# Performance work log

Measured on AMD Instinct MI355X. Metric: run time of the kernel, lower is better.

Reference implementation:

```python
import jax, jax.numpy as jnp
import numpy as np
import math

N_EMBD = 64
HEAD_SIZE = 64
B, T = 16, 2048


def setup_inputs() -> dict:
    key = jax.random.key(0)
    k1, k2, k3, k4 = jax.random.split(key, 4)
    inputs = jax.random.normal(k1, (B, T, N_EMBD), dtype=jnp.float32)
    # Causal mask: True where attention is NOT allowed (upper triangle),
    # matching masked_fill_(mask, -1e9) with mask = ~tril.
    mask = jnp.triu(jnp.ones((T, T), dtype=bool), k=1)
    # nn.Linear(n_embd, head_size, bias=False) weights, stored as
    # (n_embd, head_size) so projection is inputs @ W (== x @ W_torch.T).
    scale = 1.0 / math.sqrt(N_EMBD)
    Wq = jax.random.uniform(k2, (N_EMBD, HEAD_SIZE), jnp.float32, -scale, scale)
    Wk = jax.random.uniform(k3, (N_EMBD, HEAD_SIZE), jnp.float32, -scale, scale)
    Wv = jax.random.uniform(k4, (N_EMBD, HEAD_SIZE), jnp.float32, -scale, scale)
    return {"inputs": inputs, "mask": mask, "Wq": Wq, "Wk": Wk, "Wv": Wv}


def reference(inputs, mask, Wq, Wk, Wv):
    # inputs: (B, T, n_embd); mask: (T, T) bool broadcast over batch
    q = inputs @ Wq  # (B, T, H)
    k = inputs @ Wk  # (B, T, H)
    v = inputs @ Wv  # (B, T, H)
    inv_sqrt_h = 1.0 / math.sqrt(HEAD_SIZE)
    scores = jnp.einsum('bth,bsh->bts', q, k) * inv_sqrt_h  # (B, T, T)
    scores = jnp.where(mask, jnp.float32(-1e9), scores)
    attention = jax.nn.softmax(scores, axis=-1)
    out = jnp.einsum('bts,bsh->bth', attention, v)  # (B, T, H)
    return out
```

## Files before the change

### kernel.cpp

```cpp
#include <hip/hip_runtime.h>
#include <stdint.h>


typedef __bf16 bf16x8 __attribute__((ext_vector_type(8)));
typedef __bf16 bf16x4 __attribute__((ext_vector_type(4)));
typedef float f32x4 __attribute__((ext_vector_type(4)));

#define QSCALE 0.18033688011112042f

__device__ __forceinline__ unsigned short f2bf(float f) {
  union { float f; unsigned u; } x; x.f = f;
  unsigned r = x.u + 0x7fffu + ((x.u >> 16) & 1u);
  return (unsigned short)(r >> 16);
}

__device__ __forceinline__ int swz(int row, int bytecol) {
  return row * 128 + (bytecol ^ ((row & 7) << 4));
}
__device__ __forceinline__ bf16x8 frag(const unsigned short* base, int row, int kf, int lane) {
  int off = swz(row, kf * 64 + ((lane >> 4) << 4));
  return *(const bf16x8*)((const char*)base + off);
}

__global__ __launch_bounds__(256, 3) void proj_kernel(
    const float* __restrict__ X, const float* __restrict__ Wq,
    const float* __restrict__ Wk, const float* __restrict__ Wv,
    unsigned short* __restrict__ Qg, unsigned short* __restrict__ Kg,
    unsigned short* __restrict__ Vtg) {
  __shared__ __align__(16) unsigned short Xs[128 * 64];
  __shared__ __align__(16) unsigned short Ws[64 * 64];
  const int tid = threadIdx.x, lane = tid & 63, w = tid >> 6;
  const int mat = blockIdx.y;
  const long grow0 = (long)blockIdx.x * 128;

  for (int c = tid; c < 1024; c += 256) {
    int r = c >> 3, cc = c & 7;
    const float* src = X + (grow0 + r) * 64 + cc * 8;
    float4 f0 = *(const float4*)src;
    float4 f1 = *(const float4*)(src + 4);
    uint4 d;
    d.x = f2bf(f0.x) | ((unsigned)f2bf(f0.y) << 16);
    d.y = f2bf(f0.z) | ((unsigned)f2bf(f0.w) << 16);
    d.z = f2bf(f1.x) | ((unsigned)f2bf(f1.y) << 16);
    d.w = f2bf(f1.z) | ((unsigned)f2bf(f1.w) << 16);
    *(uint4*)((char*)Xs + swz(r, cc * 16)) = d;
  }
  const float* wsrc = (mat == 0) ? Wq : (mat == 1) ? Wk : Wv;
  for (int c = tid; c < 4096; c += 256) {
    int e = c >> 6, hh = c & 63;
    *(unsigned short*)((char*)Ws + swz(hh, e * 2)) = f2bf(wsrc[c]);
  }
  __syncthreads();

  const f32x4 zero = {0.f, 0.f, 0.f, 0.f};
  const int mrowb = w * 32;

  bf16x8 xf[2][2];
#pragma unroll
  for (int s = 0; s < 2; ++s)
#pragma unroll
    for (int kf = 0; kf < 2; ++kf)
      xf[s][kf] = frag(Xs, mrowb + s * 16 + (lane & 15), kf, lane);

  if (mat < 2) {
    unsigned short* dst = mat ? Kg : Qg;
#pragma unroll
    for (int s = 0; s < 2; ++s) {
#pragma unroll
      for (int nt = 0; nt < 4; ++nt) {
        bf16x8 b0 = frag(Ws, nt * 16 + (lane & 15), 0, lane);
        bf16x8 b1 = frag(Ws, nt * 16 + (lane & 15), 1, lane);
        f32x4 acc = __builtin_amdgcn_mfma_f32_16x16x32_bf16(xf[s][0], b0, zero, 0, 0, 0);
        acc = __builtin_amdgcn_mfma_f32_16x16x32_bf16(xf[s][1], b1, acc, 0, 0, 0);
        long row0 = grow0 + mrowb + s * 16 + ((lane >> 4) << 2);
        int col = nt * 16 + (lane & 15);
#pragma unroll
        for (int i = 0; i < 4; ++i) {
          float v = acc[i];
          if (mat == 0) v *= QSCALE;
          dst[(row0 + i) * 64 + col] = f2bf(v);
        }
      }
    }
  } else {
    const int b = (int)(grow0 >> 11);
    const int tin0 = (int)(grow0 & 2047);
#pragma unroll
    for (int mt = 0; mt < 4; ++mt) {
      bf16x8 a0 = frag(Ws, mt * 16 + (lane & 15), 0, lane);
      bf16x8 a1 = frag(Ws, mt * 16 + (lane & 15), 1, lane);
#pragma unroll
      for (int s = 0; s < 2; ++s) {
        f32x4 acc = __builtin_amdgcn_mfma_f32_16x16x32_bf16(a0, xf[s][0], zero, 0, 0, 0);
        acc = __builtin_amdgcn_mfma_f32_16x16x32_bf16(a1, xf[s][1], acc, 0, 0, 0);
        int t = tin0 + mrowb + s * 16 + (lane & 15);
        int h0 = mt * 16 + ((lane >> 4) << 2);
#pragma unroll
        for (int i = 0; i < 4; ++i)
          Vtg[((long)(b * 64 + h0 + i)) * 2048 + t] = f2bf(acc[i]);
      }
    }
  }
}

__global__ __launch_bounds__(256, 2) void attn5_kernel(
    const unsigned short* __restrict__ Qg, const unsigned short* __restrict__ Kg,
    const unsigned short* __restrict__ Vtg, float* __restrict__ Og) {
  __shared__ __align__(16) unsigned char smem[35840];

  const int bid = blockIdx.x;
  const int slot = bid >> 3;
  const int b = ((bid & 7) << 1) + (slot & 1);
  const int m = slot >> 1;
  const int qt = (slot & 1) ? (31 - m) : m;
  const int q0 = qt * 64;
  const int ns = qt + 1;

  const int tid = threadIdx.x;
  const int lane = tid & 63, w = tid >> 6;
  const int g = lane >> 4, ln = lane & 15;
  const int h = w & 1, qh = w >> 1;

  const unsigned short* qrow = Qg + ((long)b * 2048 + q0 + qh * 32) * 64;
  const bf16x8 qb00 = *(const bf16x8*)(qrow + ln * 64 + g * 8);
  const bf16x8 qb01 = *(const bf16x8*)(qrow + ln * 64 + 32 + g * 8);
  const bf16x8 qb10 = *(const bf16x8*)(qrow + (16 + ln) * 64 + g * 8);
  const bf16x8 qb11 = *(const bf16x8*)(qrow + (16 + ln) * 64 + 32 + g * 8);

  const unsigned short* kbase = Kg + (long)b * 2048 * 64;
  const unsigned short* vbase = Vtg + (long)b * 64 * 2048;

  const int sr = tid >> 2;
  const int sc = tid & 3;

  const f32x4 zero = {0.f, 0.f, 0.f, 0.f};
  f32x4 o0[4], o1[4];
#pragma unroll
  for (int nt = 0; nt < 4; ++nt) { o0[nt] = zero; o1[nt] = zero; }
  float den0 = 0.f, den1 = 0.f;

  {
    const unsigned short* kg = kbase + (long)sr * 64 + sc * 16;
    uint4 k0 = *(const uint4*)kg;
    uint4 k1 = *(const uint4*)(kg + 8);
    const unsigned short* vg = vbase + (long)sr * 2048 + sc * 16;
    uint4 v0 = *(const uint4*)vg;
    uint4 v1 = *(const uint4*)(vg + 8);
    unsigned short* Kb = (unsigned short*)smem;
    unsigned short* Vb = (unsigned short*)(smem + 8192);
    *(uint4*)((char*)Kb + swz(sr, sc * 32)) = k0;
    *(uint4*)((char*)Kb + swz(sr, sc * 32 + 16)) = k1;
    *(uint4*)((char*)Vb + swz(sr, sc * 32)) = v0;
    *(uint4*)((char*)Vb + swz(sr, sc * 32 + 16)) = v1;
  }
  __syncthreads();

  int cur = 0;
  for (int t = 0; t < ns; ++t) {
    const int kv0 = t * 64;
    const bool pre = (t + 1 < ns);
    uint4 k0, k1, v0, v1;
    if (pre) {
      const int kv0n = kv0 + 64;
      const unsigned short* kg = kbase + (long)(kv0n + sr) * 64 + sc * 16;
      k0 = *(const uint4*)kg;
      k1 = *(const uint4*)(kg + 8);
      const unsigned short* vg = vbase + (long)sr * 2048 + kv0n + sc * 16;
      v0 = *(const uint4*)vg;
      v1 = *(const uint4*)(vg + 8);
    }

    const unsigned short* Kb = (const unsigned short*)(smem + cur * 16384);
    const unsigned short* Vb = (const unsigned short*)(smem + cur * 16384 + 8192);

    bf16x8 ka00 = frag(Kb, h * 32 + ln,      0, lane);
    bf16x8 ka01 = frag(Kb, h * 32 + ln,      1, lane);
    bf16x8 ka10 = frag(Kb, h * 32 + 16 + ln, 0, lane);
    bf16x8 ka11 = frag(Kb, h * 32 + 16 + ln, 1, lane);

    bf16x8 vb[4];
#pragma unroll
    for (int nt = 0; nt < 4; ++nt) {
      int row = nt * 16 + ln;
      bf16x4 lo = *(const bf16x4*)((const char*)Vb + swz(row, h * 64 + g * 8));
      bf16x4 hi = *(const bf16x4*)((const char*)Vb + swz(row, h * 64 + 32 + g * 8));
      vb[nt] = __builtin_shufflevector(lo, hi, 0, 1, 2, 3, 4, 5, 6, 7);
    }

    __builtin_amdgcn_s_setprio(1);
    f32x4 st00 = __builtin_amdgcn_mfma_f32_16x16x32_bf16(ka00, qb00, zero, 0, 0, 0);
    st00 = __builtin_amdgcn_mfma_f32_16x16x32_bf16(ka01, qb01, st00, 0, 0, 0);
    f32x4 st01 = __builtin_amdgcn_mfma_f32_16x16x32_bf16(ka00, qb10, zero, 0, 0, 0);
    st01 = __builtin_amdgcn_mfma_f32_16x16x32_bf16(ka01, qb11, st01, 0, 0, 0);
    f32x4 st10 = __builtin_amdgcn_mfma_f32_16x16x32_bf16(ka10, qb00, zero, 0, 0, 0);
    st10 = __builtin_amdgcn_mfma_f32_16x16x32_bf16(ka11, qb01, st10, 0, 0, 0);
    f32x4 st11 = __builtin_amdgcn_mfma_f32_16x16x32_bf16(ka10, qb10, zero, 0, 0, 0);
    st11 = __builtin_amdgcn_mfma_f32_16x16x32_bf16(ka11, qb11, st11, 0, 0, 0);
    __builtin_amdgcn_s_setprio(0);

    if (t == ns - 1) {
      const int qg0 = q0 + qh * 32 + ln;
      const int qg1 = qg0 + 16;
      const int kvb = kv0 + h * 32 + g * 4;
#pragma unroll
      for (int i = 0; i < 4; ++i) {
        if (kvb + i > qg0)      st00[i] = -1e30f;
        if (kvb + i > qg1)      st01[i] = -1e30f;
        if (kvb + 16 + i > qg0) st10[i] = -1e30f;
        if (kvb + 16 + i > qg1) st11[i] = -1e30f;
      }
    }

    bf16x8 pa0, pa1;
#pragma unroll
    for (int i = 0; i < 4; ++i) {
      float p00 = exp2f(st00[i]);
      float p10 = exp2f(st10[i]);
      float p01 = exp2f(st01[i]);
      float p11 = exp2f(st11[i]);
      den0 += p00 + p10;
      den1 += p01 + p11;
      pa0[i] = (__bf16)p00;  pa0[4 + i] = (__bf16)p10;
      pa1[i] = (__bf16)p01;  pa1[4 + i] = (__bf16)p11;
    }

    __builtin_amdgcn_s_setprio(1);
#pragma unroll
    for (int nt = 0; nt < 4; ++nt) {
      o0[nt] = __builtin_amdgcn_mfma_f32_16x16x32_bf16(pa0, vb[nt], o0[nt], 0, 0, 0);
      o1[nt] = __builtin_amdgcn_mfma_f32_16x16x32_bf16(pa1, vb[nt], o1[nt], 0, 0, 0);
    }
    __builtin_amdgcn_s_setprio(0);

    if (pre) {
      unsigned short* Kn = (unsigned short*)(smem + (cur ^ 1) * 16384);
      unsigned short* Vn = (unsigned short*)(smem + (cur ^ 1) * 16384 + 8192);
      *(uint4*)((char*)Kn + swz(sr, sc * 32)) = k0;
      *(uint4*)((char*)Kn + swz(sr, sc * 32 + 16)) = k1;
      *(uint4*)((char*)Vn + swz(sr, sc * 32)) = v0;
      *(uint4*)((char*)Vn + swz(sr, sc * 32 + 16)) = v1;
    }
    __syncthreads();
    cur ^= 1;
  }

  den0 += __shfl_xor(den0, 16);
  den0 += __shfl_xor(den0, 32);
  den1 += __shfl_xor(den1, 16);
  den1 += __shfl_xor(den1, 32);

  float* Olds = (float*)smem;
  float* Dlds = (float*)(smem + 34816);
#pragma unroll
  for (int nt = 0; nt < 4; ++nt)
#pragma unroll
    for (int i = 0; i < 4; ++i) {
      Olds[(h * 64 + qh * 32 + g * 4 + i) * 68 + nt * 16 + ln] = o0[nt][i];
      Olds[(h * 64 + qh * 32 + 16 + g * 4 + i) * 68 + nt * 16 + ln] = o1[nt][i];
    }
  if (lane < 16) {
    Dlds[h * 64 + qh * 32 + ln] = den0;
    Dlds[h * 64 + qh * 32 + 16 + ln] = den1;
  }
  __syncthreads();

  const int q = tid >> 2;
  const int d0 = (tid & 3) * 16;
  float dd = Dlds[q] + Dlds[64 + q];
  float inv = 1.0f / dd;
  float acc[16];
#pragma unroll
  for (int e = 0; e < 16; ++e)
    acc[e] = (Olds[q * 68 + d0 + e] + Olds[(64 + q) * 68 + d0 + e]) * inv;
  float* outp = Og + ((long)b * 2048 + q0 + q) * 64 + d0;
#pragma unroll
  for (int v4 = 0; v4 < 4; ++v4)
    *(float4*)(outp + v4 * 4) = make_float4(acc[v4 * 4], acc[v4 * 4 + 1],
                                            acc[v4 * 4 + 2], acc[v4 * 4 + 3]);
}

extern "C" void kernel_launch(void* const* d_in, const int* in_sizes, int n_in,
                              void* d_out, int out_size, void* d_ws, size_t ws_size,
                              hipStream_t stream) {
  const float* X  = (const float*)d_in[0];
  const float* Wq = (const float*)d_in[2];
  const float* Wk = (const float*)d_in[3];
  const float* Wv = (const float*)d_in[4];

  unsigned short* Qg  = (unsigned short*)d_ws;
  unsigned short* Kg  = Qg + 2097152;
  unsigned short* Vtg = Kg + 2097152;

  proj_kernel<<<dim3(256, 3), 256, 0, stream>>>(X, Wq, Wk, Wv, Qg, Kg, Vtg);
  attn5_kernel<<<512, 256, 0, stream>>>(Qg, Kg, Vtg, (float*)d_out);
}
```

Baseline: 45.71 us.

## Widen attention KV tiles to 128 with 8 warps; fuse Q/K/V projections per block

The attention kernel now runs 512 threads per block. It stages 128-key K/V tiles, double-buffered in a 64KB LDS region, and splits each tile into four 32-key slices across warps. A two-phase LDS reduction combines the four partial outputs and denominators. This halves the number of loop iterations and barriers per query tile and adds warps to hide latency. The cost is more LDS per block, which may limit occupancy, and extra fully masked work on the last tile. The projection kernel now loads each 64-row X tile once and computes Q, K and V from it, instead of launching one block per matrix and reloading X for each.

```diff
diff --git a/kernel.cpp b/kernel.cpp
--- a/kernel.cpp
+++ b/kernel.cpp
@@ -7,6 +7,7 @@
 typedef float f32x4 __attribute__((ext_vector_type(4)));
 
 #define QSCALE 0.18033688011112042f
+#define MFMA16(a, b, c) __builtin_amdgcn_mfma_f32_16x16x32_bf16((a), (b), (c), 0, 0, 0)
 
 __device__ __forceinline__ unsigned short f2bf(float f) {
   union { float f; unsigned u; } x; x.f = f;
@@ -17,109 +18,115 @@
 __device__ __forceinline__ int swz(int row, int bytecol) {
   return row * 128 + (bytecol ^ ((row & 7) << 4));
 }
+__device__ __forceinline__ int swzV(int row, int bytecol) {
+  return row * 256 + (bytecol ^ ((row & 7) << 4));
+}
 __device__ __forceinline__ bf16x8 frag(const unsigned short* base, int row, int kf, int lane) {
   int off = swz(row, kf * 64 + ((lane >> 4) << 4));
   return *(const bf16x8*)((const char*)base + off);
 }
 
-__global__ __launch_bounds__(256, 3) void proj_kernel(
+__global__ __launch_bounds__(256, 2) void proj_kernel(
     const float* __restrict__ X, const float* __restrict__ Wq,
     const float* __restrict__ Wk, const float* __restrict__ Wv,
     unsigned short* __restrict__ Qg, unsigned short* __restrict__ Kg,
     unsigned short* __restrict__ Vtg) {
-  __shared__ __align__(16) unsigned short Xs[128 * 64];
-  __shared__ __align__(16) unsigned short Ws[64 * 64];
+  __shared__ __align__(16) unsigned short Xs[64 * 64];
+  __shared__ __align__(16) unsigned short Ws[3 * 64 * 64];
   const int tid = threadIdx.x, lane = tid & 63, w = tid >> 6;
-  const int mat = blockIdx.y;
-  const long grow0 = (long)blockIdx.x * 128;
-
-  for (int c = tid; c < 1024; c += 256) {
-    int r = c >> 3, cc = c & 7;
-    const float* src = X + (grow0 + r) * 64 + cc * 8;
+  const int ln = lane & 15, g = lane >> 4;
+  const long grow0 = (long)blockIdx.x * 64;
+  const int b = (int)(grow0 >> 11);
+  const int tin0 = (int)(grow0 & 2047);
+
+  {
+    const int r = tid >> 2, c = tid & 3;
+    const float* src = X + (grow0 + r) * 64 + c * 16;
     float4 f0 = *(const float4*)src;
     float4 f1 = *(const float4*)(src + 4);
-    uint4 d;
-    d.x = f2bf(f0.x) | ((unsigned)f2bf(f0.y) << 16);
-    d.y = f2bf(f0.z) | ((unsigned)f2bf(f0.w) << 16);
-    d.z = f2bf(f1.x) | ((unsigned)f2bf(f1.y) << 16);
-    d.w = f2bf(f1.z) | ((unsigned)f2bf(f1.w) << 16);
-    *(uint4*)((char*)Xs + swz(r, cc * 16)) = d;
-  }
-  const float* wsrc = (mat == 0) ? Wq : (mat == 1) ? Wk : Wv;
-  for (int c = tid; c < 4096; c += 256) {
-    int e = c >> 6, hh = c & 63;
-    *(unsigned short*)((char*)Ws + swz(hh, e * 2)) = f2bf(wsrc[c]);
+    float4 f2 = *(const float4*)(src + 8);
+    float4 f3 = *(const float4*)(src + 12);
+    uint4 d0, d1;
+    d0.x = f2bf(f0.x) | ((unsigned)f2bf(f0.y) << 16);
+    d0.y = f2bf(f0.z) | ((unsigned)f2bf(f0.w) << 16);
+    d0.z = f2bf(f1.x) | ((unsigned)f2bf(f1.y) << 16);
+    d0.w = f2bf(f1.z) | ((unsigned)f2bf(f1.w) << 16);
+    d1.x = f2bf(f2.x) | ((unsigned)f2bf(f2.y) << 16);
+    d1.y = f2bf(f2.z) | ((unsigned)f2bf(f2.w) << 16);
+    d1.z = f2bf(f3.x) | ((unsigned)f2bf(f3.y) << 16);
+    d1.w = f2bf(f3.z) | ((unsigned)f2bf(f3.w) << 16);
+    *(uint4*)((char*)Xs + swz(r, c * 32)) = d0;
+    *(uint4*)((char*)Xs + swz(r, c * 32 + 16)) = d1;
+  }
+  for (int c = tid; c < 3 * 4096; c += 256) {
+    const int mat = c >> 12, rr = c & 4095;
+    const int e = rr >> 6, hh = rr & 63;
+    const float* wsrc = (mat == 0) ? Wq : (mat == 1) ? Wk : Wv;
+    *(unsigned short*)((char*)(Ws + mat * 4096) + swz(hh, e * 2)) = f2bf(wsrc[rr]);
   }
   __syncthreads();
 
   const f32x4 zero = {0.f, 0.f, 0.f, 0.f};
-  const int mrowb = w * 32;
-
-  bf16x8 xf[2][2];
-#pragma unroll
-  for (int s = 0; s < 2; ++s)
-#pragma unroll
-    for (int kf = 0; kf < 2; ++kf)
-      xf[s][kf] = frag(Xs, mrowb + s * 16 + (lane & 15), kf, lane);
-
-  if (mat < 2) {
-    unsigned short* dst = mat ? Kg : Qg;
-#pragma unroll
-    for (int s = 0; s < 2; ++s) {
+#pragma unroll
+  for (int i = 0; i < 3; ++i) {
+    const int task = w * 3 + i;
+    const int mat = task >> 2, s = task & 3;
+    const unsigned short* wbase = Ws + mat * 4096;
+    if (mat < 2) {
+      bf16x8 a0 = frag(Xs, s * 16 + ln, 0, lane);
+      bf16x8 a1 = frag(Xs, s * 16 + ln, 1, lane);
+      unsigned short* dst = mat ? Kg : Qg;
 #pragma unroll
       for (int nt = 0; nt < 4; ++nt) {
-        bf16x8 b0 = frag(Ws, nt * 16 + (lane & 15), 0, lane);
-        bf16x8 b1 = frag(Ws, nt * 16 + (lane & 15), 1, lane);
-        f32x4 acc = __builtin_amdgcn_mfma_f32_16x16x32_bf16(xf[s][0], b0, zero, 0, 0, 0);
-        acc = __builtin_amdgcn_mfma_f32_16x16x32_bf16(xf[s][1], b1, acc, 0, 0, 0);
-        long row0 = grow0 + mrowb + s * 16 + ((lane >> 4) << 2);
-        int col = nt * 16 + (lane & 15);
-#pragma unroll
-        for (int i = 0; i < 4; ++i) {
-          float v = acc[i];
+        bf16x8 b0 = frag(wbase, nt * 16 + ln, 0, lane);
+        bf16x8 b1 = frag(wbase, nt * 16 + ln, 1, lane);
+        f32x4 acc = MFMA16(a0, b0, zero);
+        acc = MFMA16(a1, b1, acc);
+        long row0 = grow0 + s * 16 + g * 4;
+        int col = nt * 16 + ln;
+#pragma unroll
+        for (int k = 0; k < 4; ++k) {
+          float v = acc[k];
           if (mat == 0) v *= QSCALE;
-          dst[(row0 + i) * 64 + col] = f2bf(v);
+          dst[(row0 + k) * 64 + col] = f2bf(v);
         }
       }
-    }
-  } else {
-    const int b = (int)(grow0 >> 11);
-    const int tin0 = (int)(grow0 & 2047);
-#pragma unroll
-    for (int mt = 0; mt < 4; ++mt) {
-      bf16x8 a0 = frag(Ws, mt * 16 + (lane & 15), 0, lane);
-      bf16x8 a1 = frag(Ws, mt * 16 + (lane & 15), 1, lane);
-#pragma unroll
-      for (int s = 0; s < 2; ++s) {
-        f32x4 acc = __builtin_amdgcn_mfma_f32_16x16x32_bf16(a0, xf[s][0], zero, 0, 0, 0);
-        acc = __builtin_amdgcn_mfma_f32_16x16x32_bf16(a1, xf[s][1], acc, 0, 0, 0);
-        int t = tin0 + mrowb + s * 16 + (lane & 15);
-        int h0 = mt * 16 + ((lane >> 4) << 2);
-#pragma unroll
-        for (int i = 0; i < 4; ++i)
-          Vtg[((long)(b * 64 + h0 + i)) * 2048 + t] = f2bf(acc[i]);
+    } else {
+      bf16x8 a0 = frag(wbase, s * 16 + ln, 0, lane);
+      bf16x8 a1 = frag(wbase, s * 16 + ln, 1, lane);
+#pragma unroll
+      for (int nt = 0; nt < 4; ++nt) {
+        bf16x8 b0 = frag(Xs, nt * 16 + ln, 0, lane);
+        bf16x8 b1 = frag(Xs, nt * 16 + ln, 1, lane);
+        f32x4 acc = MFMA16(a0, b0, zero);
+        acc = MFMA16(a1, b1, acc);
+        int t = tin0 + nt * 16 + ln;
+        int h0 = s * 16 + g * 4;
+#pragma unroll
+        for (int k = 0; k < 4; ++k)
+          Vtg[((long)(b * 64 + h0 + k)) * 2048 + t] = f2bf(acc[k]);
       }
     }
   }
 }
 
-__global__ __launch_bounds__(256, 2) void attn5_kernel(
+__global__ __launch_bounds__(512, 4) void attn7_kernel(
     const unsigned short* __restrict__ Qg, const unsigned short* __restrict__ Kg,
     const unsigned short* __restrict__ Vtg, float* __restrict__ Og) {
-  __shared__ __align__(16) unsigned char smem[35840];
+  __shared__ __align__(16) unsigned char smem[65536];
 
   const int bid = blockIdx.x;
-  const int slot = bid >> 3;
-  const int b = ((bid & 7) << 1) + (slot & 1);
-  const int m = slot >> 1;
-  const int qt = (slot & 1) ? (31 - m) : m;
+  const int xcd = bid & 7, idx = bid >> 3;
+  const int b = (xcd << 1) + (idx & 1);
+  const int m = idx >> 1;
+  const int qt = (idx & 1) ? (31 - m) : m;
   const int q0 = qt * 64;
-  const int ns = qt + 1;
+  const int ns = (qt >> 1) + 1;
 
   const int tid = threadIdx.x;
   const int lane = tid & 63, w = tid >> 6;
   const int g = lane >> 4, ln = lane & 15;
-  const int h = w & 1, qh = w >> 1;
+  const int kvq = w & 3, qh = w >> 2;
 
   const unsigned short* qrow = Qg + ((long)b * 2048 + q0 + qh * 32) * 64;
   const bf16x8 qb00 = *(const bf16x8*)(qrow + ln * 64 + g * 8);
@@ -130,8 +137,8 @@
   const unsigned short* kbase = Kg + (long)b * 2048 * 64;
   const unsigned short* vbase = Vtg + (long)b * 64 * 2048;
 
-  const int sr = tid >> 2;
-  const int sc = tid & 3;
+  const int rk = tid >> 2, ck = tid & 3;
+  const int rv = tid >> 3, cv = tid & 7;
 
   const f32x4 zero = {0.f, 0.f, 0.f, 0.f};
   f32x4 o0[4], o1[4];
@@ -140,68 +147,64 @@
   float den0 = 0.f, den1 = 0.f;
 
   {
-    const unsigned short* kg = kbase + (long)sr * 64 + sc * 16;
+    const unsigned short* kg = kbase + (long)rk * 64 + ck * 16;
     uint4 k0 = *(const uint4*)kg;
     uint4 k1 = *(const uint4*)(kg + 8);
-    const unsigned short* vg = vbase + (long)sr * 2048 + sc * 16;
+    const unsigned short* vg = vbase + (long)rv * 2048 + cv * 16;
     uint4 v0 = *(const uint4*)vg;
     uint4 v1 = *(const uint4*)(vg + 8);
-    unsigned short* Kb = (unsigned short*)smem;
-    unsigned short* Vb = (unsigned short*)(smem + 8192);
-    *(uint4*)((char*)Kb + swz(sr, sc * 32)) = k0;
-    *(uint4*)((char*)Kb + swz(sr, sc * 32 + 16)) = k1;
-    *(uint4*)((char*)Vb + swz(sr, sc * 32)) = v0;
-    *(uint4*)((char*)Vb + swz(sr, sc * 32 + 16)) = v1;
+    unsigned char* Kb = smem;
+    unsigned char* Vb = smem + 16384;
+    *(uint4*)(Kb + swz(rk, ck * 32)) = k0;
+    *(uint4*)(Kb + swz(rk, ck * 32 + 16)) = k1;
+    *(uint4*)(Vb + swzV(rv, cv * 32)) = v0;
+    *(uint4*)(Vb + swzV(rv, cv * 32 + 16)) = v1;
   }
   __syncthreads();
 
   int cur = 0;
   for (int t = 0; t < ns; ++t) {
-    const int kv0 = t * 64;
+    const int kv0 = t * 128;
     const bool pre = (t + 1 < ns);
     uint4 k0, k1, v0, v1;
     if (pre) {
-      const int kv0n = kv0 + 64;
-      const unsigned short* kg = kbase + (long)(kv0n + sr) * 64 + sc * 16;
+      const int kv0n = kv0 + 128;
+      const unsigned short* kg = kbase + (long)(kv0n + rk) * 64 + ck * 16;
       k0 = *(const uint4*)kg;
       k1 = *(const uint4*)(kg + 8);
-      const unsigned short* vg = vbase + (long)sr * 2048 + kv0n + sc * 16;
+      const unsigned short* vg = vbase + (long)rv * 2048 + kv0n + cv * 16;
       v0 = *(const uint4*)vg;
       v1 = *(const uint4*)(vg + 8);
     }
 
-    const unsigned short* Kb = (const unsigned short*)(smem + cur * 16384);
-    const unsigned short* Vb = (const unsigned short*)(smem + cur * 16384 + 8192);
-
-    bf16x8 ka00 = frag(Kb, h * 32 + ln,      0, lane);
-    bf16x8 ka01 = frag(Kb, h * 32 + ln,      1, lane);
-    bf16x8 ka10 = frag(Kb, h * 32 + 16 + ln, 0, lane);
-    bf16x8 ka11 = frag(Kb, h * 32 + 16 + ln, 1, lane);
+    const unsigned short* Kb = (const unsigned short*)(smem + cur * 32768);
+    const unsigned char*  Vb = smem + cur * 32768 + 16384;
+
+    bf16x8 ka00 = frag(Kb, kvq * 32 + ln,      0, lane);
+    bf16x8 ka01 = frag(Kb, kvq * 32 + ln,      1, lane);
+    bf16x8 ka10 = frag(Kb, kvq * 32 + 16 + ln, 0, lane);
+    bf16x8 ka11 = frag(Kb, kvq * 32 + 16 + ln, 1, lane);
 
     bf16x8 vb[4];
 #pragma unroll
     for (int nt = 0; nt < 4; ++nt) {
       int row = nt * 16 + ln;
-      bf16x4 lo = *(const bf16x4*)((const char*)Vb + swz(row, h * 64 + g * 8));
-      bf16x4 hi = *(const bf16x4*)((const char*)Vb + swz(row, h * 64 + 32 + g * 8));
+      bf16x4 lo = *(const bf16x4*)(Vb + swzV(row, kvq * 64 + g * 8));
+      bf16x4 hi = *(const bf16x4*)(Vb + swzV(row, kvq * 64 + 32 + g * 8));
       vb[nt] = __builtin_shufflevector(lo, hi, 0, 1, 2, 3, 4, 5, 6, 7);
     }
 
     __builtin_amdgcn_s_setprio(1);
-    f32x4 st00 = __builtin_amdgcn_mfma_f32_16x16x32_bf16(ka00, qb00, zero, 0, 0, 0);
-    st00 = __builtin_amdgcn_mfma_f32_16x16x32_bf16(ka01, qb01, st00, 0, 0, 0);
-    f32x4 st01 = __builtin_amdgcn_mfma_f32_16x16x32_bf16(ka00, qb10, zero, 0, 0, 0);
-    st01 = __builtin_amdgcn_mfma_f32_16x16x32_bf16(ka01, qb11, st01, 0, 0, 0);
-    f32x4 st10 = __builtin_amdgcn_mfma_f32_16x16x32_bf16(ka10, qb00, zero, 0, 0, 0);
-    st10 = __builtin_amdgcn_mfma_f32_16x16x32_bf16(ka11, qb01, st10, 0, 0, 0);
-    f32x4 st11 = __builtin_amdgcn_mfma_f32_16x16x32_bf16(ka10, qb10, zero, 0, 0, 0);
-    st11 = __builtin_amdgcn_mfma_f32_16x16x32_bf16(ka11, qb11, st11, 0, 0, 0);
+    f32x4 st00 = MFMA16(ka00, qb00, zero);  st00 = MFMA16(ka01, qb01, st00);
+    f32x4 st01 = MFMA16(ka00, qb10, zero);  st01 = MFMA16(ka01, qb11, st01);
+    f32x4 st10 = MFMA16(ka10, qb00, zero);  st10 = MFMA16(ka11, qb01, st10);
+    f32x4 st11 = MFMA16(ka10, qb10, zero);  st11 = MFMA16(ka11, qb11, st11);
     __builtin_amdgcn_s_setprio(0);
 
     if (t == ns - 1) {
       const int qg0 = q0 + qh * 32 + ln;
       const int qg1 = qg0 + 16;
-      const int kvb = kv0 + h * 32 + g * 4;
+      const int kvb = kv0 + kvq * 32 + g * 4;
 #pragma unroll
       for (int i = 0; i < 4; ++i) {
         if (kvb + i > qg0)      st00[i] = -1e30f;
@@ -227,18 +230,18 @@
     __builtin_amdgcn_s_setprio(1);
 #pragma unroll
     for (int nt = 0; nt < 4; ++nt) {
-      o0[nt] = __builtin_amdgcn_mfma_f32_16x16x32_bf16(pa0, vb[nt], o0[nt], 0, 0, 0);
-      o1[nt] = __builtin_amdgcn_mfma_f32_16x16x32_bf16(pa1, vb[nt], o1[nt], 0, 0, 0);
+      o0[nt] = MFMA16(pa0, vb[nt], o0[nt]);
+      o1[nt] = MFMA16(pa1, vb[nt], o1[nt]);
     }
     __builtin_amdgcn_s_setprio(0);
 
     if (pre) {
-      unsigned short* Kn = (unsigned short*)(smem + (cur ^ 1) * 16384);
-      unsigned short* Vn = (unsigned short*)(smem + (cur ^ 1) * 16384 + 8192);
-      *(uint4*)((char*)Kn + swz(sr, sc * 32)) = k0;
-      *(uint4*)((char*)Kn + swz(sr, sc * 32 + 16)) = k1;
-      *(uint4*)((char*)Vn + swz(sr, sc * 32)) = v0;
-      *(uint4*)((char*)Vn + swz(sr, sc * 32 + 16)) = v1;
+      unsigned char* Kn = smem + (cur ^ 1) * 32768;
+      unsigned char* Vn = Kn + 16384;
+      *(uint4*)(Kn + swz(rk, ck * 32)) = k0;
+      *(uint4*)(Kn + swz(rk, ck * 32 + 16)) = k1;
+      *(uint4*)(Vn + swzV(rv, cv * 32)) = v0;
+      *(uint4*)(Vn + swzV(rv, cv * 32 + 16)) = v1;
     }
     __syncthreads();
     cur ^= 1;
@@ -251,32 +254,39 @@
 
   float* Olds = (float*)smem;
   float* Dlds = (float*)(smem + 34816);
-#pragma unroll
-  for (int nt = 0; nt < 4; ++nt)
-#pragma unroll
-    for (int i = 0; i < 4; ++i) {
-      Olds[(h * 64 + qh * 32 + g * 4 + i) * 68 + nt * 16 + ln] = o0[nt][i];
-      Olds[(h * 64 + qh * 32 + 16 + g * 4 + i) * 68 + nt * 16 + ln] = o1[nt][i];
-    }
   if (lane < 16) {
-    Dlds[h * 64 + qh * 32 + ln] = den0;
-    Dlds[h * 64 + qh * 32 + 16 + ln] = den1;
-  }
-  __syncthreads();
-
-  const int q = tid >> 2;
-  const int d0 = (tid & 3) * 16;
-  float dd = Dlds[q] + Dlds[64 + q];
-  float inv = 1.0f / dd;
-  float acc[16];
-#pragma unroll
-  for (int e = 0; e < 16; ++e)
-    acc[e] = (Olds[q * 68 + d0 + e] + Olds[(64 + q) * 68 + d0 + e]) * inv;
-  float* outp = Og + ((long)b * 2048 + q0 + q) * 64 + d0;
-#pragma unroll
-  for (int v4 = 0; v4 < 4; ++v4)
-    *(float4*)(outp + v4 * 4) = make_float4(acc[v4 * 4], acc[v4 * 4 + 1],
-                                            acc[v4 * 4 + 2], acc[v4 * 4 + 3]);
+    Dlds[kvq * 64 + qh * 32 + ln] = den0;
+    Dlds[kvq * 64 + qh * 32 + 16 + ln] = den1;
+  }
+#pragma unroll
+  for (int phase = 0; phase < 2; ++phase) {
+    if (phase) __syncthreads();
+    if (qh == phase) {
+#pragma unroll
+      for (int nt = 0; nt < 4; ++nt)
+#pragma unroll
+        for (int i = 0; i < 4; ++i) {
+          Olds[(kvq * 32 + g * 4 + i) * 68 + nt * 16 + ln] = o0[nt][i];
+          Olds[(kvq * 32 + 16 + g * 4 + i) * 68 + nt * 16 + ln] = o1[nt][i];
+        }
+    }
+    __syncthreads();
+    const int q = tid >> 4;
+    const int d0 = (tid & 15) * 4;
+    const int qq = phase * 32 + q;
+    float dd = Dlds[qq] + Dlds[64 + qq] + Dlds[128 + qq] + Dlds[192 + qq];
+    float inv = 1.0f / dd;
+    float4 r0 = *(float4*)&Olds[(0 * 32 + q) * 68 + d0];
+    float4 r1 = *(float4*)&Olds[(1 * 32 + q) * 68 + d0];
+    float4 r2 = *(float4*)&Olds[(2 * 32 + q) * 68 + d0];
+    float4 r3 = *(float4*)&Olds[(3 * 32 + q) * 68 + d0];
+    float4 out;
+    out.x = (r0.x + r1.x + r2.x + r3.x) * inv;
+    out.y = (r0.y + r1.y + r2.y + r3.y) * inv;
+    out.z = (r0.z + r1.z + r2.z + r3.z) * inv;
+    out.w = (r0.w + r1.w + r2.w + r3.w) * inv;
+    *(float4*)(Og + ((long)b * 2048 + q0 + qq) * 64 + d0) = out;
+  }
 }
 
 extern "C" void kernel_launch(void* const* d_in, const int* in_sizes, int n_in,
@@ -291,6 +301,6 @@
   unsigned short* Kg  = Qg + 2097152;
   unsigned short* Vtg = Kg + 2097152;
 
-  proj_kernel<<<dim3(256, 3), 256, 0, stream>>>(X, Wq, Wk, Wv, Qg, Kg, Vtg);
-  attn5_kernel<<<512, 256, 0, stream>>>(Qg, Kg, Vtg, (float*)d_out);
-}
+  proj_kernel<<<512, 256, 0, stream>>>(X, Wq, Wk, Wv, Qg, Kg, Vtg);
+  attn7_kernel<<<512, 512, 0, stream>>>(Qg, Kg, Vtg, (float*)d_out);
+}
```

After: 46.85 us. +2.5%, slower.

## Fuse Q/K/V projections into one block per 256-row tile

Applied to the files above, without the earlier changes.

The projection kernel now has each block load a 256-row tile of X once and compute all three projections from it, instead of launching a separate block per matrix that reloads the same X tile. This cuts redundant global reads and fp32-to-bf16 conversion of X, at the cost of 128 blocks instead of 768, more shared memory per block, and lower occupancy. The attention kernel changes only cosmetically through an MFMA macro.

```diff
diff --git a/kernel.cpp b/kernel.cpp
--- a/kernel.cpp
+++ b/kernel.cpp
@@ -7,6 +7,7 @@
 typedef float f32x4 __attribute__((ext_vector_type(4)));
 
 #define QSCALE 0.18033688011112042f
+#define MFMA16(a, b, c) __builtin_amdgcn_mfma_f32_16x16x32_bf16((a), (b), (c), 0, 0, 0)
 
 __device__ __forceinline__ unsigned short f2bf(float f) {
   union { float f; unsigned u; } x; x.f = f;
@@ -22,83 +23,88 @@
   return *(const bf16x8*)((const char*)base + off);
 }
 
-__global__ __launch_bounds__(256, 3) void proj_kernel(
+__global__ __launch_bounds__(256, 2) void proj_kernel(
     const float* __restrict__ X, const float* __restrict__ Wq,
     const float* __restrict__ Wk, const float* __restrict__ Wv,
     unsigned short* __restrict__ Qg, unsigned short* __restrict__ Kg,
     unsigned short* __restrict__ Vtg) {
-  __shared__ __align__(16) unsigned short Xs[128 * 64];
-  __shared__ __align__(16) unsigned short Ws[64 * 64];
+  __shared__ __align__(16) unsigned short Xs[256 * 64];
+  __shared__ __align__(16) unsigned short Ws[3 * 64 * 64];
   const int tid = threadIdx.x, lane = tid & 63, w = tid >> 6;
-  const int mat = blockIdx.y;
-  const long grow0 = (long)blockIdx.x * 128;
-
-  for (int c = tid; c < 1024; c += 256) {
-    int r = c >> 3, cc = c & 7;
-    const float* src = X + (grow0 + r) * 64 + cc * 8;
+  const int ln = lane & 15, g = lane >> 4;
+  const long grow0 = (long)blockIdx.x * 256;
+  const int b = (int)(grow0 >> 11);
+  const int tin0 = (int)(grow0 & 2047);
+
+#pragma unroll
+  for (int pass = 0; pass < 4; ++pass) {
+    const int r = pass * 64 + (tid >> 2), c = tid & 3;
+    const float* src = X + (grow0 + r) * 64 + c * 16;
     float4 f0 = *(const float4*)src;
     float4 f1 = *(const float4*)(src + 4);
-    uint4 d;
-    d.x = f2bf(f0.x) | ((unsigned)f2bf(f0.y) << 16);
-    d.y = f2bf(f0.z) | ((unsigned)f2bf(f0.w) << 16);
-    d.z = f2bf(f1.x) | ((unsigned)f2bf(f1.y) << 16);
-    d.w = f2bf(f1.z) | ((unsigned)f2bf(f1.w) << 16);
-    *(uint4*)((char*)Xs + swz(r, cc * 16)) = d;
-  }
-  const float* wsrc = (mat == 0) ? Wq : (mat == 1) ? Wk : Wv;
-  for (int c = tid; c < 4096; c += 256) {
-    int e = c >> 6, hh = c & 63;
-    *(unsigned short*)((char*)Ws + swz(hh, e * 2)) = f2bf(wsrc[c]);
+    float4 f2 = *(const float4*)(src + 8);
+    float4 f3 = *(const float4*)(src + 12);
+    uint4 d0, d1;
+    d0.x = f2bf(f0.x) | ((unsigned)f2bf(f0.y) << 16);
+    d0.y = f2bf(f0.z) | ((unsigned)f2bf(f0.w) << 16);
+    d0.z = f2bf(f1.x) | ((unsigned)f2bf(f1.y) << 16);
+    d0.w = f2bf(f1.z) | ((unsigned)f2bf(f1.w) << 16);
+    d1.x = f2bf(f2.x) | ((unsigned)f2bf(f2.y) << 16);
+    d1.y = f2bf(f2.z) | ((unsigned)f2bf(f2.w) << 16);
+    d1.z = f2bf(f3.x) | ((unsigned)f2bf(f3.y) << 16);
+    d1.w = f2bf(f3.z) | ((unsigned)f2bf(f3.w) << 16);
+    *(uint4*)((char*)Xs + swz(r, c * 32)) = d0;
+    *(uint4*)((char*)Xs + swz(r, c * 32 + 16)) = d1;
+  }
+  for (int c = tid; c < 3 * 4096; c += 256) {
+    const int mat = c >> 12, rr = c & 4095;
+    const int e = rr >> 6, hh = rr & 63;
+    const float* wsrc = (mat == 0) ? Wq : (mat == 1) ? Wk : Wv;
+    *(unsigned short*)((char*)(Ws + mat * 4096) + swz(hh, e * 2)) = f2bf(wsrc[rr]);
   }
   __syncthreads();
 
   const f32x4 zero = {0.f, 0.f, 0.f, 0.f};
-  const int mrowb = w * 32;
-
-  bf16x8 xf[2][2];
-#pragma unroll
-  for (int s = 0; s < 2; ++s)
-#pragma unroll
-    for (int kf = 0; kf < 2; ++kf)
-      xf[s][kf] = frag(Xs, mrowb + s * 16 + (lane & 15), kf, lane);
-
-  if (mat < 2) {
-    unsigned short* dst = mat ? Kg : Qg;
-#pragma unroll
-    for (int s = 0; s < 2; ++s) {
+  const int rbase = w * 64;
+
+#pragma unroll
+  for (int s = 0; s < 4; ++s) {
+    const int xrow = rbase + s * 16;
+    bf16x8 a0 = frag(Xs, xrow + ln, 0, lane);
+    bf16x8 a1 = frag(Xs, xrow + ln, 1, lane);
+#pragma unroll
+    for (int mat = 0; mat < 2; ++mat) {
+      unsigned short* dst = mat ? Kg : Qg;
+      const unsigned short* wbase = Ws + mat * 4096;
 #pragma unroll
       for (int nt = 0; nt < 4; ++nt) {
-        bf16x8 b0 = frag(Ws, nt * 16 + (lane & 15), 0, lane);
-        bf16x8 b1 = frag(Ws, nt * 16 + (lane & 15), 1, lane);
-        f32x4 acc = __builtin_amdgcn_mfma_f32_16x16x32_bf16(xf[s][0], b0, zero, 0, 0, 0);
-        acc = __builtin_amdgcn_mfma_f32_16x16x32_bf16(xf[s][1], b1, acc, 0, 0, 0);
-        long row0 = grow0 + mrowb + s * 16 + ((lane >> 4) << 2);
-        int col = nt * 16 + (lane & 15);
-#pragma unroll
-        for (int i = 0; i < 4; ++i) {
-          float v = acc[i];
+        bf16x8 b0 = frag(wbase, nt * 16 + ln, 0, lane);
+        bf16x8 b1 = frag(wbase, nt * 16 + ln, 1, lane);
+        f32x4 acc = MFMA16(a0, b0, zero);
+        acc = MFMA16(a1, b1, acc);
+        long row0 = grow0 + xrow + g * 4;
+        int col = nt * 16 + ln;
+#pragma unroll
+        for (int k = 0; k < 4; ++k) {
+          float v = acc[k];
           if (mat == 0) v *= QSCALE;
-          dst[(row0 + i) * 64 + col] = f2bf(v);
+          dst[(row0 + k) * 64 + col] = f2bf(v);
         }
       }
     }
-  } else {
-    const int b = (int)(grow0 >> 11);
-    const int tin0 = (int)(grow0 & 2047);
+    const unsigned short* wv = Ws + 2 * 4096;
+    bf16x8 xb0 = a0, xb1 = a1;
 #pragma unroll
     for (int mt = 0; mt < 4; ++mt) {
-      bf16x8 a0 = frag(Ws, mt * 16 + (lane & 15), 0, lane);
-      bf16x8 a1 = frag(Ws, mt * 16 + (lane & 15), 1, lane);
-#pragma unroll
-      for (int s = 0; s < 2; ++s) {
-        f32x4 acc = __builtin_amdgcn_mfma_f32_16x16x32_bf16(a0, xf[s][0], zero, 0, 0, 0);
-        acc = __builtin_amdgcn_mfma_f32_16x16x32_bf16(a1, xf[s][1], acc, 0, 0, 0);
-        int t = tin0 + mrowb + s * 16 + (lane & 15);
-        int h0 = mt * 16 + ((lane >> 4) << 2);
-#pragma unroll
-        for (int i = 0; i < 4; ++i)
-          Vtg[((long)(b * 64 + h0 + i)) * 2048 + t] = f2bf(acc[i]);
-      }
+      bf16x8 wa0 = frag(wv, mt * 16 + ln, 0, lane);
+      bf16x8 wa1 = frag(wv, mt * 16 + ln, 1, lane);
+      f32x4 acc = MFMA16(wa0, xb0, zero);
+      acc = MFMA16(wa1, xb1, acc);
+      int t = tin0 + xrow + ln;
+      int h0 = mt * 16 + g * 4;
+#pragma unroll
+      for (int k = 0; k < 4; ++k)
+        Vtg[((long)(b * 64 + h0 + k)) * 2048 + t] = f2bf(acc[k]);
     }
   }
 }
@@ -188,14 +194,10 @@
     }
 
     __builtin_amdgcn_s_setprio(1);
-    f32x4 st00 = __builtin_amdgcn_mfma_f32_16x16x32_bf16(ka00, qb00, zero, 0, 0, 0);
-    st00 = __builtin_amdgcn_mfma_f32_16x16x32_bf16(ka01, qb01, st00, 0, 0, 0);
-    f32x4 st01 = __builtin_amdgcn_mfma_f32_16x16x32_bf16(ka00, qb10, zero, 0, 0, 0);
-    st01 = __builtin_amdgcn_mfma_f32_16x16x32_bf16(ka01, qb11, st01, 0, 0, 0);
-    f32x4 st10 = __builtin_amdgcn_mfma_f32_16x16x32_bf16(ka10, qb00, zero, 0, 0, 0);
-    st10 = __builtin_amdgcn_mfma_f32_16x16x32_bf16(ka11, qb01, st10, 0, 0, 0);
-    f32x4 st11 = __builtin_amdgcn_mfma_f32_16x16x32_bf16(ka10, qb10, zero, 0, 0, 0);
-    st11 = __builtin_amdgcn_mfma_f32_16x16x32_bf16(ka11, qb11, st11, 0, 0, 0);
+    f32x4 st00 = MFMA16(ka00, qb00, zero);  st00 = MFMA16(ka01, qb01, st00);
+    f32x4 st01 = MFMA16(ka00, qb10, zero);  st01 = MFMA16(ka01, qb11, st01);
+    f32x4 st10 = MFMA16(ka10, qb00, zero);  st10 = MFMA16(ka11, qb01, st10);
+    f32x4 st11 = MFMA16(ka10, qb10, zero);  st11 = MFMA16(ka11, qb11, st11);
     __builtin_amdgcn_s_setprio(0);
 
     if (t == ns - 1) {
@@ -227,8 +229,8 @@
     __builtin_amdgcn_s_setprio(1);
 #pragma unroll
     for (int nt = 0; nt < 4; ++nt) {
-      o0[nt] = __builtin_amdgcn_mfma_f32_16x16x32_bf16(pa0, vb[nt], o0[nt], 0, 0, 0);
-      o1[nt] = __builtin_amdgcn_mfma_f32_16x16x32_bf16(pa1, vb[nt], o1[nt], 0, 0, 0);
+      o0[nt] = MFMA16(pa0, vb[nt], o0[nt]);
+      o1[nt] = MFMA16(pa1, vb[nt], o1[nt]);
     }
     __builtin_amdgcn_s_setprio(0);
 
@@ -291,6 +293,6 @@
   unsigned short* Kg  = Qg + 2097152;
   unsigned short* Vtg = Kg + 2097152;
 
-  proj_kernel<<<dim3(256, 3), 256, 0, stream>>>(X, Wq, Wk, Wv, Qg, Kg, Vtg);
+  proj_kernel<<<128, 256, 0, stream>>>(X, Wq, Wk, Wv, Qg, Kg, Vtg);
   attn5_kernel<<<512, 256, 0, stream>>>(Qg, Kg, Vtg, (float*)d_out);
 }
```

Result: slower. 50.06 us (+9.5%).
